# Kernel optimization log

Hardware: AMD Instinct MI355X
Metric: run time of the kernel (lower is better)

Reference implementation:

```python
import jax, jax.numpy as jnp
import numpy as np

N_DOMAINS = 8
LN_EPS = 1e-5


def setup_inputs() -> dict:
    key = jax.random.key(0)
    ks = jax.random.split(key, 4)
    N, D_IN, D_HID, D_OUT = 32768, 256, 1024, 256
    x = jax.random.normal(ks[0], (N, D_IN), dtype=jnp.float32)
    domain_types = jax.random.randint(ks[1], (N,), 0, N_DOMAINS, dtype=jnp.int32)
    # Per-domain MLP parameters (8 independent experts)
    W1 = jax.random.normal(ks[2], (N_DOMAINS, D_IN, D_HID), dtype=jnp.float32) * (1.0 / np.sqrt(D_IN))
    b1 = jnp.zeros((N_DOMAINS, D_HID), dtype=jnp.float32)
    gamma = jnp.ones((N_DOMAINS, D_HID), dtype=jnp.float32)
    beta = jnp.zeros((N_DOMAINS, D_HID), dtype=jnp.float32)
    W2 = jax.random.normal(ks[3], (N_DOMAINS, D_HID, D_OUT), dtype=jnp.float32) * (1.0 / np.sqrt(D_HID))
    b2 = jnp.zeros((N_DOMAINS, D_OUT), dtype=jnp.float32)
    return {"x": x, "domain_types": domain_types, "W1": W1, "b1": b1,
            "gamma": gamma, "beta": beta, "W2": W2, "b2": b2}


def _expert_mlp(x, W1d, b1d, gd, bd, W2d, b2d):
    # Linear -> LayerNorm -> ReLU -> (Dropout: identity at eval) -> Linear
    h = x @ W1d + b1d                       # [N, hid]
    mu = jnp.mean(h, axis=-1, keepdims=True)
    var = jnp.mean(jnp.square(h - mu), axis=-1, keepdims=True)
    h = (h - mu) * jax.lax.rsqrt(var + LN_EPS) * gd + bd
    h = jax.nn.relu(h)
    return h @ W2d + b2d                    # [N, out]


def reference(x, domain_types, W1, b1, gamma, beta, W2, b2):
    # output dim == x.shape[-1] (as in the torch code: zeros(batch, x.shape[-1]))
    out = jnp.zeros((x.shape[0], x.shape[-1]), dtype=x.dtype)
    for d in range(N_DOMAINS):  # small fixed expert loop (static MoE dispatch)
        y = _expert_mlp(x, W1[d], b1[d], gamma[d], beta[d], W2[d], b2[d])
        mask = (domain_types == d)[:, None]
        out = jnp.where(mask, y, out)
    return out
```

## Files before the change

kernel.cpp:

```cpp
#include <hip/hip_runtime.h>
#include <hip/hip_bf16.h>


#define ND 8
#define NROWS 32768
#define DIN 256
#define DHID 1024
#define DOUT 256
#define MPAD 33792
#define NTILES 264

typedef short short8 __attribute__((ext_vector_type(8)));
typedef float floatx4 __attribute__((ext_vector_type(4)));

__device__ __forceinline__ unsigned short f2bf(float f) {
    unsigned u = __builtin_bit_cast(unsigned, f);
    unsigned r = u + 0x7fff + ((u >> 16) & 1);
    return (unsigned short)(r >> 16);
}
__device__ __forceinline__ float bf2f(unsigned short h) {
    unsigned u = ((unsigned)h) << 16;
    return __builtin_bit_cast(float, u);
}

#define GLDS16(gp, lp) __builtin_amdgcn_global_load_lds( \
    (const __attribute__((address_space(1))) void*)(gp), \
    (__attribute__((address_space(3))) void*)(lp), 16, 0, 0)

__global__ void transpose_both(const float* __restrict__ W1, unsigned short* __restrict__ W1T,
                               const float* __restrict__ W2, unsigned short* __restrict__ W2T,
                               int* __restrict__ cnt) {
    if (blockIdx.x == 0 && threadIdx.x < 16) cnt[threadIdx.x] = 0;
    __shared__ float t[32][33];
    int b = blockIdx.x;
    const float* in; unsigned short* out; int R, C, bx, by, z;
    if (b < 2048) {
        in = W1; out = W1T; R = DIN; C = DHID;
        bx = b & 31; by = (b >> 5) & 7; z = b >> 8;
    } else {
        b -= 2048;
        in = W2; out = W2T; R = DHID; C = DOUT;
        bx = b & 7; by = (b >> 3) & 31; z = b >> 8;
    }
    const int c0 = bx * 32, r0 = by * 32;
    const int tx = threadIdx.x & 31, ty = threadIdx.x >> 5;
    const float* src = in + (size_t)z * R * C;
    unsigned short* dst = out + (size_t)z * R * C;
#pragma unroll
    for (int i = 0; i < 32; i += 8)
        t[ty + i][tx] = src[(size_t)(r0 + ty + i) * C + c0 + tx];
    __syncthreads();
#pragma unroll
    for (int i = 0; i < 32; i += 8)
        dst[(size_t)(c0 + ty + i) * R + r0 + tx] = f2bf(t[tx][ty + i]);
}

__global__ void init_histo(const int* __restrict__ dt, int* __restrict__ perm,
                           int* __restrict__ counts) {
    const int i = blockIdx.x * 256 + threadIdx.x;
    if (i < MPAD) perm[i] = -1;
    __shared__ int lc[ND];
    if (threadIdx.x < ND) lc[threadIdx.x] = 0;
    __syncthreads();
    if (i < NROWS) atomicAdd(&lc[dt[i]], 1);
    __syncthreads();
    if (threadIdx.x < ND && lc[threadIdx.x] > 0)
        atomicAdd(&counts[threadIdx.x], lc[threadIdx.x]);
}

__global__ void make_meta(const int* __restrict__ counts, int* __restrict__ cursors,
                          int2* __restrict__ meta) {
    __shared__ int base[ND], ntc[ND];
    const int t = threadIdx.x;
    if (t == 0) {
        int off = 0;
        for (int d = 0; d < ND; d++) {
            base[d] = off;
            ntc[d] = (counts[d] + 127) >> 7;
            cursors[d] = off;
            off += ntc[d] << 7;
        }
    }
    __syncthreads();
    for (int i = t; i < NTILES; i += 64) {
        int2 m = make_int2(-1, 0);
#pragma unroll
        for (int d = 0; d < ND; d++) {
            const int ti = i - (base[d] >> 7);
            if (ti >= 0 && ti < ntc[d]) m = make_int2(d, base[d] + (ti << 7));
        }
        meta[i] = m;
    }
}

__global__ __launch_bounds__(256)
void assign_pos(const int* __restrict__ dt, int* __restrict__ cursors,
                int* __restrict__ perm, int* __restrict__ pos) {
    __shared__ int lcnt[ND];
    __shared__ int lbase[ND];
    const int tid = threadIdx.x;
    if (tid < ND) lcnt[tid] = 0;
    __syncthreads();
    const int r = blockIdx.x * 256 + tid;
    const int d = dt[r];
    const int myrank = atomicAdd(&lcnt[d], 1);
    __syncthreads();
    if (tid < ND && lcnt[tid] > 0)
        lbase[tid] = atomicAdd(&cursors[tid], lcnt[tid]);
    __syncthreads();
    const int p = lbase[d] + myrank;
    pos[r] = p;
    perm[p] = r;
}

__global__ __launch_bounds__(256)
void copy_rows(const float* __restrict__ x, const int* __restrict__ pos,
               unsigned short* __restrict__ xs) {
    const int tid = threadIdx.x;
    const int lane = tid & 63;
    const int r = blockIdx.x * 4 + (tid >> 6);
    const int p = pos[r];
    float4 v = ((const float4*)(x + (size_t)r * DIN))[lane];
    ushort4 o;
    o.x = f2bf(v.x); o.y = f2bf(v.y); o.z = f2bf(v.z); o.w = f2bf(v.w);
    ((ushort4*)(xs + (size_t)p * DIN))[lane] = o;
}

template <int K, bool ISB>
__global__ __launch_bounds__(256, 2)
void gemm_bt(const unsigned short* __restrict__ A,
             const unsigned short* __restrict__ Bt,
             const float* __restrict__ bias,
             const int2* __restrict__ meta,
             const int* __restrict__ perm,
             unsigned short* __restrict__ Cbf,
             float* __restrict__ Cf,
             const int Ntot,
             float2* __restrict__ spart,
             const float* __restrict__ gamma,
             const float* __restrict__ beta) {
    const int2 md = meta[blockIdx.x];
    const int dom = md.x;
    if (dom < 0) return;
    const int m0 = md.y;
    const int n0 = blockIdx.y * 128;

    __shared__ unsigned short As[128 * 32];
    __shared__ unsigned short Bs[128 * 32];
    __shared__ float sred[2][128];

    const int tid = threadIdx.x;
    const int lane = tid & 63;
    const int w = tid >> 6;
    const int wr = w >> 1, wc = w & 1;

    const unsigned short* Abase = A + (size_t)m0 * K;
    const unsigned short* Bbase = Bt + (size_t)dom * Ntot * K + (size_t)n0 * K;

    if (!ISB) {
        if (tid < 128) { sred[0][tid] = 0.f; sred[1][tid] = 0.f; }
    }

    const int ma = (w * 128 + lane) >> 2;
    const int kc = lane & 3;
    float muv[2], rsv[2];
    short8 hv0{}, hv1{};
    float4 gc0{}, gc1{}, ec0{}, ec1{};
    if (ISB) {
#pragma unroll
        for (int h2 = 0; h2 < 2; ++h2) {
            const int rm = m0 + ma + h2 * 16;
            float s = 0.f, s2 = 0.f;
#pragma unroll
            for (int nb = 0; nb < 8; ++nb) {
                const float2 p = spart[(size_t)nb * MPAD + rm];
                s += p.x; s2 += p.y;
            }
            const float mu = s * (1.f / 1024.f);
            const float var = fmaxf(s2 * (1.f / 1024.f) - mu * mu, 0.f);
            muv[h2] = mu;
            rsv[h2] = rsqrtf(var + 1e-5f);
        }
        const float* gp = gamma + dom * DHID + kc * 8;
        const float* bp = beta + dom * DHID + kc * 8;
        gc0 = ((const float4*)gp)[0]; gc1 = ((const float4*)gp)[1];
        ec0 = ((const float4*)bp)[0]; ec1 = ((const float4*)bp)[1];
        hv0 = *(const short8*)(Abase + (size_t)ma * K + kc * 8);
        hv1 = *(const short8*)(Abase + (size_t)(ma + 16) * K + kc * 8);
    }

    floatx4 acc[4][4];
#pragma unroll
    for (int i = 0; i < 4; i++)
#pragma unroll
        for (int j = 0; j < 4; j++) acc[i][j] = 0.f;

    for (int k0 = 0; k0 < K; k0 += 32) {
#pragma unroll
        for (int it = 0; it < 2; ++it) {
            const int c = w * 128 + it * 64 + lane;
            const int m = c >> 2, kcc = c & 3;
            GLDS16(Bbase + (size_t)m * K + k0 + kcc * 8, &Bs[(w * 128 + it * 64) * 8]);
        }
        if (!ISB) {
#pragma unroll
            for (int it = 0; it < 2; ++it) {
                const int c = w * 128 + it * 64 + lane;
                const int m = c >> 2, kcc = c & 3;
                GLDS16(Abase + (size_t)m * K + k0 + kcc * 8, &As[(w * 128 + it * 64) * 8]);
            }
        } else {
            const float gA[8] = {gc0.x, gc0.y, gc0.z, gc0.w, gc1.x, gc1.y, gc1.z, gc1.w};
            const float eA[8] = {ec0.x, ec0.y, ec0.z, ec0.w, ec1.x, ec1.y, ec1.z, ec1.w};
#pragma unroll
            for (int h2 = 0; h2 < 2; ++h2) {
                const float mu = muv[h2], rs = rsv[h2];
                const short8 hvv = h2 ? hv1 : hv0;
                short8 o;
#pragma unroll
                for (int e = 0; e < 8; ++e) {
                    const float rg = gA[e] * rs;
                    const float v = fmaxf(fmaf(bf2f((unsigned short)hvv[e]), rg,
                                               fmaf(-mu, rg, eA[e])), 0.f);
                    o[e] = (short)f2bf(v);
                }
                *(short8*)&As[(w * 128 + h2 * 64 + lane) * 8] = o;
            }
        }
        __syncthreads();

        short8 nh0{}, nh1{};
        float4 ng0{}, ng1{}, ne0{}, ne1{};
        const bool more = ISB && (k0 + 32 < K);
        if (more) {
            const float* gp = gamma + dom * DHID + k0 + 32 + kc * 8;
            const float* bp = beta + dom * DHID + k0 + 32 + kc * 8;
            ng0 = ((const float4*)gp)[0]; ng1 = ((const float4*)gp)[1];
            ne0 = ((const float4*)bp)[0]; ne1 = ((const float4*)bp)[1];
            nh0 = *(const short8*)(Abase + (size_t)ma * K + k0 + 32 + kc * 8);
            nh1 = *(const short8*)(Abase + (size_t)(ma + 16) * K + k0 + 32 + kc * 8);
        }

        short8 a[4], b[4];
        const int kk = (lane >> 4) * 8;
#pragma unroll
        for (int i = 0; i < 4; i++) {
            const int m = wr * 64 + i * 16 + (lane & 15);
            a[i] = *(const short8*)&As[m * 32 + kk];
            const int n = wc * 64 + i * 16 + (lane & 15);
            b[i] = *(const short8*)&Bs[n * 32 + kk];
        }
#pragma unroll
        for (int i = 0; i < 4; i++)
#pragma unroll
            for (int j = 0; j < 4; j++)
                acc[i][j] = __builtin_amdgcn_mfma_f32_16x16x32_bf16(a[i], b[j], acc[i][j], 0, 0, 0);
        __syncthreads();

        if (more) { hv0 = nh0; hv1 = nh1; gc0 = ng0; gc1 = ng1; ec0 = ne0; ec1 = ne1; }
    }

    const int quad = lane >> 4;
    const int l15 = lane & 15;
    if (!ISB) {
        float bv[4];
#pragma unroll
        for (int j = 0; j < 4; j++)
            bv[j] = bias[dom * Ntot + n0 + wc * 64 + j * 16 + l15];
#pragma unroll
        for (int i = 0; i < 4; i++) {
#pragma unroll
            for (int r = 0; r < 4; r++) {
                const int rl = wr * 64 + i * 16 + quad * 4 + r;
                float s = 0.f, s2 = 0.f;
#pragma unroll
                for (int j = 0; j < 4; j++) {
                    const float v = acc[i][j][r] + bv[j];
                    Cbf[(size_t)(m0 + rl) * Ntot + n0 + wc * 64 + j * 16 + l15] = f2bf(v);
                    s += v; s2 += v * v;
                }
#pragma unroll
                for (int o = 8; o; o >>= 1) {
                    s  += __shfl_xor(s, o, 64);
                    s2 += __shfl_xor(s2, o, 64);
                }
                if (l15 == 0) {
                    atomicAdd(&sred[0][rl], s);
                    atomicAdd(&sred[1][rl], s2);
                }
            }
        }
        __syncthreads();
        if (tid < 128)
            spart[(size_t)blockIdx.y * MPAD + m0 + tid] =
                make_float2(sred[0][tid], sred[1][tid]);
    } else {
#pragma unroll
        for (int i = 0; i < 4; i++) {
            const int rowbase = m0 + wr * 64 + i * 16 + quad * 4;
#pragma unroll
            for (int r = 0; r < 4; r++) {
                const int orig = perm[rowbase + r];
                if (orig < 0) continue;
#pragma unroll
                for (int j = 0; j < 4; j++) {
                    const int col = n0 + wc * 64 + j * 16 + l15;
                    Cf[(size_t)orig * Ntot + col] = acc[i][j][r] + bias[dom * Ntot + col];
                }
            }
        }
    }
}

extern "C" void kernel_launch(void* const* d_in, const int* in_sizes, int n_in,
                              void* d_out, int out_size, void* d_ws, size_t ws_size,
                              hipStream_t stream) {
    const float* x = (const float*)d_in[0];
    const int* dt = (const int*)d_in[1];
    const float* W1 = (const float*)d_in[2];
    const float* b1 = (const float*)d_in[3];
    const float* gamma = (const float*)d_in[4];
    const float* beta = (const float*)d_in[5];
    const float* W2 = (const float*)d_in[6];
    const float* b2 = (const float*)d_in[7];
    float* out = (float*)d_out;

    char* ws = (char*)d_ws;
    size_t off = 0;
    auto take = [&](size_t nbytes) -> char* {
        char* p = ws + off;
        off = (off + nbytes + 255) & ~(size_t)255;
        return p;
    };
    unsigned short* W1T = (unsigned short*)take((size_t)ND * DHID * DIN * 2);
    unsigned short* W2T = (unsigned short*)take((size_t)ND * DOUT * DHID * 2);
    unsigned short* XS  = (unsigned short*)take((size_t)MPAD * DIN * 2);
    unsigned short* H   = (unsigned short*)take((size_t)MPAD * DHID * 2);
    float2* SPART = (float2*)take((size_t)8 * MPAD * 8);
    int* PERM   = (int*)take(MPAD * 4);
    int* POS    = (int*)take(NROWS * 4);
    int* CNT    = (int*)take(64);
    int2* META  = (int2*)take(NTILES * 8);
    (void)ws_size; (void)n_in; (void)in_sizes; (void)out_size;

    int* COUNTS = CNT;
    int* CURSORS = CNT + 8;

    transpose_both<<<4096, 256, 0, stream>>>(W1, W1T, W2, W2T, CNT);
    init_histo<<<MPAD / 256, 256, 0, stream>>>(dt, PERM, COUNTS);
    make_meta<<<1, 64, 0, stream>>>(COUNTS, CURSORS, META);
    assign_pos<<<NROWS / 256, 256, 0, stream>>>(dt, CURSORS, PERM, POS);
    copy_rows<<<NROWS / 4, 256, 0, stream>>>(x, POS, XS);
    gemm_bt<DIN, false><<<dim3(NTILES, DHID / 128), 256, 0, stream>>>(
        XS, W1T, b1, META, nullptr, H, nullptr, DHID, SPART, nullptr, nullptr);
    gemm_bt<DHID, true><<<dim3(NTILES, DOUT / 128), 256, 0, stream>>>(
        H, W2T, b2, META, PERM, nullptr, out, DOUT, SPART, gamma, beta);
}
```

Before: 212.9 us.

## Double-buffer LDS tiles, remap blocks across XCDs, cache gamma/beta in LDS

The grouped GEMM kernels now use double-buffered shared-memory tiles, so the next K-slice is staged while MFMAs run on the current one. This removes one barrier per iteration. The 2D grid is flattened to 1D, and the block index is permuted so consecutive tiles land on the same XCD (bid&7 interleave), which should improve L2 reuse of weights. For the second GEMM, gamma and beta are preloaded into LDS, and s_setprio is raised around the MFMA blocks. The cost is double the LDS per block, which may reduce occupancy under the 2-blocks-per-CU launch bounds.

```diff
diff --git a/kernel.cpp b/kernel.cpp
--- a/kernel.cpp
+++ b/kernel.cpp
@@ -139,20 +139,28 @@
              float2* __restrict__ spart,
              const float* __restrict__ gamma,
              const float* __restrict__ beta) {
-    const int2 md = meta[blockIdx.x];
+    constexpr int NB = ISB ? 2 : 8;
+    constexpr int NWG = NTILES * NB;
+    constexpr int NS = K / 32;
+    const int bid = (int)blockIdx.x;
+    const int wid = (bid & 7) * (NWG >> 3) + (bid >> 3);
+    const int tile = wid / NB;
+    const int n0 = (wid % NB) * 128;
+    const int2 md = meta[tile];
     const int dom = md.x;
     if (dom < 0) return;
     const int m0 = md.y;
-    const int n0 = blockIdx.y * 128;
-
-    __shared__ unsigned short As[128 * 32];
-    __shared__ unsigned short Bs[128 * 32];
+
+    __shared__ unsigned short As[2][128 * 32];
+    __shared__ unsigned short Bs[2][128 * 32];
+    __shared__ float gb[ISB ? 2048 : 64];
     __shared__ float sred[2][128];
 
     const int tid = threadIdx.x;
     const int lane = tid & 63;
     const int w = tid >> 6;
     const int wr = w >> 1, wc = w & 1;
+    const int l15 = lane & 15;
 
     const unsigned short* Abase = A + (size_t)m0 * K;
     const unsigned short* Bbase = Bt + (size_t)dom * Ntot * K + (size_t)n0 * K;
@@ -165,8 +173,9 @@
     const int kc = lane & 3;
     float muv[2], rsv[2];
     short8 hv0{}, hv1{};
-    float4 gc0{}, gc1{}, ec0{}, ec1{};
     if (ISB) {
+        ((float4*)gb)[tid] = ((const float4*)(gamma + dom * DHID))[tid];
+        ((float4*)(gb + 1024))[tid] = ((const float4*)(beta + dom * DHID))[tid];
 #pragma unroll
         for (int h2 = 0; h2 < 2; ++h2) {
             const int rm = m0 + ma + h2 * 16;
@@ -181,87 +190,126 @@
             muv[h2] = mu;
             rsv[h2] = rsqrtf(var + 1e-5f);
         }
-        const float* gp = gamma + dom * DHID + kc * 8;
-        const float* bp = beta + dom * DHID + kc * 8;
-        gc0 = ((const float4*)gp)[0]; gc1 = ((const float4*)gp)[1];
-        ec0 = ((const float4*)bp)[0]; ec1 = ((const float4*)bp)[1];
         hv0 = *(const short8*)(Abase + (size_t)ma * K + kc * 8);
         hv1 = *(const short8*)(Abase + (size_t)(ma + 16) * K + kc * 8);
     }
 
+#define STAGE_B(buf, t_) {                                                     \
+        const int k0_ = (t_) * 32;                                             \
+        _Pragma("unroll")                                                      \
+        for (int it = 0; it < 2; ++it) {                                       \
+            const int c = w * 128 + it * 64 + lane;                            \
+            const int m_ = c >> 2, kcc = c & 3;                                \
+            GLDS16(Bbase + (size_t)m_ * K + k0_ + kcc * 8,                     \
+                   &Bs[buf][(w * 128 + it * 64) * 8]);                         \
+        }                                                                      \
+    }
+#define STAGE_A_GLDS(buf, t_) {                                                \
+        const int k0_ = (t_) * 32;                                             \
+        _Pragma("unroll")                                                      \
+        for (int it = 0; it < 2; ++it) {                                       \
+            const int c = w * 128 + it * 64 + lane;                            \
+            const int m_ = c >> 2, kcc = c & 3;                                \
+            GLDS16(Abase + (size_t)m_ * K + k0_ + kcc * 8,                     \
+                   &As[buf][(w * 128 + it * 64) * 8]);                         \
+        }                                                                      \
+    }
+#define STAGE_A_XFRM(buf, t_) {                                                \
+        const int k1 = (t_) * 32 + kc * 8;                                     \
+        const float4 g0 = *(const float4*)&gb[k1];                             \
+        const float4 g1 = *(const float4*)&gb[k1 + 4];                         \
+        const float4 e0 = *(const float4*)&gb[1024 + k1];                      \
+        const float4 e1 = *(const float4*)&gb[1024 + k1 + 4];                  \
+        const float gA[8] = {g0.x, g0.y, g0.z, g0.w, g1.x, g1.y, g1.z, g1.w};  \
+        const float eA[8] = {e0.x, e0.y, e0.z, e0.w, e1.x, e1.y, e1.z, e1.w};  \
+        _Pragma("unroll")                                                      \
+        for (int h2 = 0; h2 < 2; ++h2) {                                       \
+            const float mu = muv[h2], rs = rsv[h2];                            \
+            const short8 hvv = h2 ? hv1 : hv0;                                 \
+            short8 o;                                                          \
+            _Pragma("unroll")                                                  \
+            for (int e = 0; e < 8; ++e) {                                      \
+                const float rg = gA[e] * rs;                                   \
+                const float v = fmaxf(fmaf(bf2f((unsigned short)hvv[e]), rg,   \
+                                           fmaf(-mu, rg, eA[e])), 0.f);        \
+                o[e] = (short)f2bf(v);                                         \
+            }                                                                  \
+            *(short8*)&As[buf][(w * 128 + h2 * 64 + lane) * 8] = o;            \
+        }                                                                      \
+    }
+#define LOAD_H(t_) {                                                           \
+        const int k0_ = (t_) * 32;                                             \
+        hv0 = *(const short8*)(Abase + (size_t)ma * K + k0_ + kc * 8);         \
+        hv1 = *(const short8*)(Abase + (size_t)(ma + 16) * K + k0_ + kc * 8);  \
+    }
+
     floatx4 acc[4][4];
 #pragma unroll
     for (int i = 0; i < 4; i++)
 #pragma unroll
         for (int j = 0; j < 4; j++) acc[i][j] = 0.f;
 
-    for (int k0 = 0; k0 < K; k0 += 32) {
-#pragma unroll
-        for (int it = 0; it < 2; ++it) {
-            const int c = w * 128 + it * 64 + lane;
-            const int m = c >> 2, kcc = c & 3;
-            GLDS16(Bbase + (size_t)m * K + k0 + kcc * 8, &Bs[(w * 128 + it * 64) * 8]);
-        }
+    STAGE_B(0, 0)
+    if (!ISB) {
+        STAGE_A_GLDS(0, 0)
+    } else {
+        STAGE_A_XFRM(0, 0)
+        LOAD_H(1)
+    }
+    __syncthreads();
+
+    int cur = 0;
+    const int kk = (lane >> 4) * 8;
+    for (int t = 0; t < NS - 1; ++t) {
+        const int nx = cur ^ 1;
+        STAGE_B(nx, t + 1)
         if (!ISB) {
-#pragma unroll
-            for (int it = 0; it < 2; ++it) {
-                const int c = w * 128 + it * 64 + lane;
-                const int m = c >> 2, kcc = c & 3;
-                GLDS16(Abase + (size_t)m * K + k0 + kcc * 8, &As[(w * 128 + it * 64) * 8]);
-            }
+            STAGE_A_GLDS(nx, t + 1)
         } else {
-            const float gA[8] = {gc0.x, gc0.y, gc0.z, gc0.w, gc1.x, gc1.y, gc1.z, gc1.w};
-            const float eA[8] = {ec0.x, ec0.y, ec0.z, ec0.w, ec1.x, ec1.y, ec1.z, ec1.w};
-#pragma unroll
-            for (int h2 = 0; h2 < 2; ++h2) {
-                const float mu = muv[h2], rs = rsv[h2];
-                const short8 hvv = h2 ? hv1 : hv0;
-                short8 o;
-#pragma unroll
-                for (int e = 0; e < 8; ++e) {
-                    const float rg = gA[e] * rs;
-                    const float v = fmaxf(fmaf(bf2f((unsigned short)hvv[e]), rg,
-                                               fmaf(-mu, rg, eA[e])), 0.f);
-                    o[e] = (short)f2bf(v);
-                }
-                *(short8*)&As[(w * 128 + h2 * 64 + lane) * 8] = o;
-            }
-        }
-        __syncthreads();
-
-        short8 nh0{}, nh1{};
-        float4 ng0{}, ng1{}, ne0{}, ne1{};
-        const bool more = ISB && (k0 + 32 < K);
-        if (more) {
-            const float* gp = gamma + dom * DHID + k0 + 32 + kc * 8;
-            const float* bp = beta + dom * DHID + k0 + 32 + kc * 8;
-            ng0 = ((const float4*)gp)[0]; ng1 = ((const float4*)gp)[1];
-            ne0 = ((const float4*)bp)[0]; ne1 = ((const float4*)bp)[1];
-            nh0 = *(const short8*)(Abase + (size_t)ma * K + k0 + 32 + kc * 8);
-            nh1 = *(const short8*)(Abase + (size_t)(ma + 16) * K + k0 + 32 + kc * 8);
-        }
-
+            STAGE_A_XFRM(nx, t + 1)
+            if (t + 2 < NS) LOAD_H(t + 2)
+        }
         short8 a[4], b[4];
-        const int kk = (lane >> 4) * 8;
 #pragma unroll
         for (int i = 0; i < 4; i++) {
-            const int m = wr * 64 + i * 16 + (lane & 15);
-            a[i] = *(const short8*)&As[m * 32 + kk];
-            const int n = wc * 64 + i * 16 + (lane & 15);
-            b[i] = *(const short8*)&Bs[n * 32 + kk];
-        }
+            const int m = wr * 64 + i * 16 + l15;
+            a[i] = *(const short8*)&As[cur][m * 32 + kk];
+            const int n = wc * 64 + i * 16 + l15;
+            b[i] = *(const short8*)&Bs[cur][n * 32 + kk];
+        }
+        __builtin_amdgcn_s_setprio(1);
 #pragma unroll
         for (int i = 0; i < 4; i++)
 #pragma unroll
             for (int j = 0; j < 4; j++)
                 acc[i][j] = __builtin_amdgcn_mfma_f32_16x16x32_bf16(a[i], b[j], acc[i][j], 0, 0, 0);
+        __builtin_amdgcn_s_setprio(0);
         __syncthreads();
-
-        if (more) { hv0 = nh0; hv1 = nh1; gc0 = ng0; gc1 = ng1; ec0 = ne0; ec1 = ne1; }
-    }
+        cur = nx;
+    }
+    {
+        short8 a[4], b[4];
+#pragma unroll
+        for (int i = 0; i < 4; i++) {
+            const int m = wr * 64 + i * 16 + l15;
+            a[i] = *(const short8*)&As[cur][m * 32 + kk];
+            const int n = wc * 64 + i * 16 + l15;
+            b[i] = *(const short8*)&Bs[cur][n * 32 + kk];
+        }
+        __builtin_amdgcn_s_setprio(1);
+#pragma unroll
+        for (int i = 0; i < 4; i++)
+#pragma unroll
+            for (int j = 0; j < 4; j++)
+                acc[i][j] = __builtin_amdgcn_mfma_f32_16x16x32_bf16(a[i], b[j], acc[i][j], 0, 0, 0);
+        __builtin_amdgcn_s_setprio(0);
+    }
+#undef STAGE_B
+#undef STAGE_A_GLDS
+#undef STAGE_A_XFRM
+#undef LOAD_H
 
     const int quad = lane >> 4;
-    const int l15 = lane & 15;
     if (!ISB) {
         float bv[4];
 #pragma unroll
@@ -292,7 +340,7 @@
         }
         __syncthreads();
         if (tid < 128)
-            spart[(size_t)blockIdx.y * MPAD + m0 + tid] =
+            spart[(size_t)(n0 >> 7) * MPAD + m0 + tid] =
                 make_float2(sred[0][tid], sred[1][tid]);
     } else {
 #pragma unroll
@@ -351,8 +399,8 @@
     make_meta<<<1, 64, 0, stream>>>(COUNTS, CURSORS, META);
     assign_pos<<<NROWS / 256, 256, 0, stream>>>(dt, CURSORS, PERM, POS);
     copy_rows<<<NROWS / 4, 256, 0, stream>>>(x, POS, XS);
-    gemm_bt<DIN, false><<<dim3(NTILES, DHID / 128), 256, 0, stream>>>(
+    gemm_bt<DIN, false><<<NTILES * 8, 256, 0, stream>>>(
         XS, W1T, b1, META, nullptr, H, nullptr, DHID, SPART, nullptr, nullptr);
-    gemm_bt<DHID, true><<<dim3(NTILES, DOUT / 128), 256, 0, stream>>>(
+    gemm_bt<DHID, true><<<NTILES * 2, 256, 0, stream>>>(
         H, W2T, b2, META, PERM, nullptr, out, DOUT, SPART, gamma, beta);
 }
```

Result: faster. 201.6 us (-5.3%).
